# Performance work log

Hardware: AMD Instinct MI355X
Metric: run time of the kernel (lower is better)

Reference implementation:

```python
import jax, jax.numpy as jnp
import numpy as np

B, S, H, D = 4, 2048, 12, 64
HID = H * D  # 768
EPS = 1e-5


def _layer_norm(h, w, b):
    mu = jnp.mean(h, axis=-1, keepdims=True)
    var = jnp.mean((h - mu) ** 2, axis=-1, keepdims=True)
    return w * (h - mu) / jnp.sqrt(var + EPS) + b


def setup_inputs() -> dict:
    key = jax.random.key(0)
    ks = jax.random.split(key, 12)
    sc = 1.0 / np.sqrt(HID)
    inp = {
        "x": jax.random.normal(ks[0], (B, S, HID), jnp.float32),
        "ln1_w": jnp.ones((HID,), jnp.float32),
        "ln1_b": jnp.zeros((HID,), jnp.float32),
        "Wq": jax.random.normal(ks[1], (HID, HID), jnp.float32) * sc,
        "bq": jnp.zeros((HID,), jnp.float32),
        "Wk": jax.random.normal(ks[2], (HID, HID), jnp.float32) * sc,
        "bk": jnp.zeros((HID,), jnp.float32),
        "Wv": jax.random.normal(ks[3], (HID, HID), jnp.float32) * sc,
        "bv": jnp.zeros((HID,), jnp.float32),
        "Wo": jax.random.normal(ks[4], (HID, HID), jnp.float32) * sc,
        "bo": jnp.zeros((HID,), jnp.float32),
        "ln2_w": jnp.ones((HID,), jnp.float32),
        "ln2_b": jnp.zeros((HID,), jnp.float32),
        "W1": jax.random.normal(ks[5], (HID, 4 * HID), jnp.float32) * sc,
        "b1": jnp.zeros((4 * HID,), jnp.float32),
        "W2": jax.random.normal(ks[6], (4 * HID, HID), jnp.float32) * (1.0 / np.sqrt(4 * HID)),
        "b2": jnp.zeros((HID,), jnp.float32),
    }
    return inp


def _split_heads(t):
    # (B, S, H*D) -> (B, H, S, D)
    b, s, _ = t.shape
    return t.reshape(b, s, H, -1).transpose(0, 2, 1, 3)


def _merge_heads(t):
    # (B, H, S, D) -> (B, S, H*D)
    b, h, s, d = t.shape
    return t.transpose(0, 2, 1, 3).reshape(b, s, h * d)


def _attention(h, Wq, bq, Wk, bk, Wv, bv, Wo, bo):
    q = _split_heads(h @ Wq + bq)  # (B,H,S,D)
    k = _split_heads(h @ Wk + bk)
    v = _split_heads(h @ Wv + bv)
    scores = jnp.einsum("bhqd,bhkd->bhqk", q, k) / jnp.sqrt(jnp.asarray(D, h.dtype))
    causal = jnp.tril(jnp.ones((q.shape[2], q.shape[2]), bool))  # (S,S)
    scores = jnp.where(causal, scores, jnp.finfo(scores.dtype).min)
    w = jax.nn.softmax(scores, axis=-1)
    out = jnp.einsum("bhqk,bhkd->bhqd", w, v)
    return _merge_heads(out) @ Wo + bo


def reference(x, ln1_w, ln1_b, Wq, bq, Wk, bk, Wv, bv, Wo, bo, ln2_w, ln2_b, W1, b1, W2, b2):
    # Pre-LN transformer block: x + attn(LN(x)); then x + MLP(LN(x))
    a = _attention(_layer_norm(x, ln1_w, ln1_b), Wq, bq, Wk, bk, Wv, bv, Wo, bo)
    x = x + a
    h = _layer_norm(x, ln2_w, ln2_b)
    m = jax.nn.gelu(h @ W1 + b1, approximate=False) @ W2 + b2
    return x + m
```

## Files before the change

kernel.cpp:

```cpp
#include <hip/hip_runtime.h>
#include <cmath>
#include <stdint.h>

typedef unsigned short u16;
typedef __attribute__((ext_vector_type(8))) short short8;
typedef __attribute__((ext_vector_type(4))) float f32x4;
typedef __attribute__((ext_vector_type(4))) unsigned int u32x4;

#define HID 768
#define FF  3072
#define SEQ 2048
#define NHEAD 12
#define NROWS 8192

__device__ __forceinline__ float bf2f(u16 u){ return __uint_as_float(((unsigned)u)<<16); }
__device__ __forceinline__ u16 f2bf(float f){
  unsigned x = __float_as_uint(f);
  x += 0x7fffu + ((x>>16)&1u);
  return (u16)(x>>16);
}
__device__ __forceinline__ unsigned pack2(float a, float b){
  return (unsigned)f2bf(a) | ((unsigned)f2bf(b) << 16);
}
__device__ __forceinline__ void gload16(const void* g, void* l){
  __builtin_amdgcn_global_load_lds((const __attribute__((address_space(1))) unsigned*)g,
                                   (__attribute__((address_space(3))) unsigned*)l, 16, 0, 0);
}

__global__ __launch_bounds__(256) void wconv(const float* __restrict__ in,
                                             u16* __restrict__ out, int K, int N)
{
  __shared__ float t[32][33];
  const int bk = blockIdx.x*32, bn = blockIdx.y*32;
  const int tn = threadIdx.x & 31, tk = threadIdx.x >> 5;
  #pragma unroll
  for (int j=0;j<4;++j)
    t[tk+8*j][tn] = in[(size_t)(bk+tk+8*j)*N + bn + tn];
  __syncthreads();
  #pragma unroll
  for (int j=0;j<4;++j)
    out[(size_t)(bn+tk+8*j)*K + bk + tn] = f2bf(t[tn][tk+8*j]);
}

__global__ __launch_bounds__(256) void tconv(const u16* __restrict__ in,
                                             u16* __restrict__ out, int K, int N)
{
  __shared__ u16 t[32][34];
  const int bk = blockIdx.x*32, bn = blockIdx.y*32;
  const int tn = threadIdx.x & 31, tk = threadIdx.x >> 5;
  #pragma unroll
  for (int j=0;j<4;++j)
    t[tk+8*j][tn] = in[(size_t)(bk+tk+8*j)*N + bn + tn];
  __syncthreads();
  #pragma unroll
  for (int j=0;j<4;++j)
    out[(size_t)(bn+tk+8*j)*K + bk + tn] = t[tn][tk+8*j];
}

__global__ __launch_bounds__(256) void ln_k(const float* __restrict__ in,
    const float* __restrict__ gw, const float* __restrict__ gb,
    u16* __restrict__ out)
{
  const int row = blockIdx.x*4 + (threadIdx.x>>6);
  const int l = threadIdx.x & 63;
  const float* p = in + (size_t)row*HID;
  float4 v[3];
  float s=0.f, ss=0.f;
  #pragma unroll
  for (int j=0;j<3;++j){
    v[j] = *(const float4*)(p + j*256 + l*4);
    s  += v[j].x + v[j].y + v[j].z + v[j].w;
    ss += v[j].x*v[j].x + v[j].y*v[j].y + v[j].z*v[j].z + v[j].w*v[j].w;
  }
  #pragma unroll
  for (int m=1;m<64;m<<=1){
    s  += __shfl_xor(s,  m, 64);
    ss += __shfl_xor(ss, m, 64);
  }
  const float mu = s * (1.f/768.f);
  const float rstd = rsqrtf(ss*(1.f/768.f) - mu*mu + 1e-5f);
  #pragma unroll
  for (int j=0;j<3;++j){
    const float4 wv = *(const float4*)(gw + j*256 + l*4);
    const float4 bv = *(const float4*)(gb + j*256 + l*4);
    ushort4 o;
    o.x = f2bf((v[j].x-mu)*rstd*wv.x + bv.x);
    o.y = f2bf((v[j].y-mu)*rstd*wv.y + bv.y);
    o.z = f2bf((v[j].z-mu)*rstd*wv.z + bv.z);
    o.w = f2bf((v[j].w-mu)*rstd*wv.w + bv.w);
    *(ushort4*)(out + (size_t)row*HID + j*256 + l*4) = o;
  }
}

template<int MODE>
__global__ __launch_bounds__(256) void gemm_bt(const u16* __restrict__ A,
    const u16* __restrict__ Bt, const float* __restrict__ bias0,
    const float* __restrict__ bias1, const float* __restrict__ bias2,
    const float* __restrict__ res, void* __restrict__ outp,
    int N, int K, long wstride, long ostride)
{
  __shared__ __align__(16) u16 sA[128*32];
  __shared__ __align__(16) u16 sB[128*32];
  const int tid = threadIdx.x, l = tid&63, w = tid>>6;
  const int wr = w>>1, wc = w&1, hi = l>>4, lo = l&15;
  const int bm = blockIdx.x*128, bn = blockIdx.y*128;
  const int z = blockIdx.z;
  const u16* Bz = Bt + (size_t)z * (size_t)wstride;
  const float* bias = (z==0) ? bias0 : ((z==1)? bias1 : bias2);

  const f32x4 zv = {0.f,0.f,0.f,0.f};
  f32x4 acc[4][4];
  #pragma unroll
  for (int i=0;i<4;++i)
    #pragma unroll
    for (int j=0;j<4;++j) acc[i][j] = zv;

  for (int kt=0; kt<K; kt+=32){
    __syncthreads();
    #pragma unroll
    for (int j=0;j<2;++j){
      int c = tid + 256*j;
      int row = c>>2, off = (c&3)*8;
      gload16(A  + (size_t)(bm + row)*K + kt + off, (char*)sA + c*16);
      gload16(Bz + (size_t)(bn + row)*K + kt + off, (char*)sB + c*16);
    }
    __syncthreads();
    short8 af[4], bfv[4];
    #pragma unroll
    for (int i=0;i<4;++i){
      af[i]  = *(const short8*)(sA + (wr*64 + i*16 + lo)*32 + hi*8);
      bfv[i] = *(const short8*)(sB + (wc*64 + i*16 + lo)*32 + hi*8);
    }
    #pragma unroll
    for (int mi=0;mi<4;++mi)
      #pragma unroll
      for (int ni=0;ni<4;++ni)
        acc[mi][ni] = __builtin_amdgcn_mfma_f32_16x16x32_bf16(af[mi], bfv[ni], acc[mi][ni], 0,0,0);
  }

  #pragma unroll
  for (int mi=0;mi<4;++mi)
    #pragma unroll
    for (int ni=0;ni<4;++ni){
      const int r0 = bm + wr*64 + mi*16 + 4*hi;
      const int cc = bn + wc*64 + ni*16 + lo;
      const float bv = bias[cc];
      #pragma unroll
      for (int g=0; g<4; ++g){
        const size_t idx = (size_t)(r0+g)*N + cc;
        float v = acc[mi][ni][g] + bv;
        if (MODE == 0){
          ((u16*)outp + (size_t)z*(size_t)ostride)[idx] = f2bf(v);
        } else if (MODE == 1){
          ((float*)outp)[idx] = res[idx] + v;
        } else {
          float gx = 0.5f*v*(1.f + erff(v*0.70710678118f));
          ((u16*)outp)[idx] = f2bf(gx);
        }
      }
    }
}

__global__ __launch_bounds__(256, 4) void attn_k(const u16* __restrict__ Qm,
                                                 const u16* __restrict__ Km,
                                                 const u16* __restrict__ Vt,
                                                 u16* __restrict__ Om)
{
  __shared__ __align__(16) u16 sK [64*64];
  __shared__ __align__(16) u16 sVT[64*64];
  const int tid = threadIdx.x, l = tid & 63, w = tid >> 6;
  const int hi = l >> 4, lo = l & 15;
  const int idx = blockIdx.x;
  const int qb = 31 - (idx / 48);
  const int bh = idx % 48;
  const int b = bh / NHEAD, h = bh - (bh / NHEAD) * NHEAD;
  const size_t rb = (size_t)b * SEQ;
  const int qw = qb*64 + w*16;

  short8 qf[2];
  #pragma unroll
  for (int ks=0; ks<2; ++ks){
    short8 t = *(const short8*)(Qm + (rb + qw + lo)*HID + h*64 + ks*32 + hi*8);
    #pragma unroll
    for (int i=0;i<8;++i) t[i] = (short)f2bf(bf2f((u16)t[i]) * 0.125f);
    qf[ks] = t;
  }

  const f32x4 zv = {0.f,0.f,0.f,0.f};
  f32x4 oa[4] = {zv, zv, zv, zv};
  float m = -INFINITY, lsum = 0.f;
  const int srcA = (((2*hi)  & 3) << 4) | lo;
  const int srcB = (((2*hi+1)& 3) << 4) | lo;

  for (int t=0; t<=qb; ++t){
    const int kv0 = t*64;
    __syncthreads();
    #pragma unroll
    for (int j=0;j<2;++j){
      int c = tid + 256*j;
      int row = c >> 3;
      int d0 = ((c&7) ^ (row&7))*8;
      gload16(Km + (rb + kv0 + row)*HID + h*64 + d0, (char*)sK + c*16);
    }
    #pragma unroll
    for (int j=0;j<2;++j){
      int c = tid + 256*j;
      int row = c >> 3;
      int k0 = ((c&7) ^ (row&7))*8;
      gload16(Vt + (size_t)(h*64 + row)*NROWS + rb + kv0 + k0, (char*)sVT + c*16);
    }
    __syncthreads();

    f32x4 sc[4] = {zv, zv, zv, zv};
    #pragma unroll
    for (int ks=0;ks<2;++ks){
      #pragma unroll
      for (int ni=0;ni<4;++ni){
        short8 kf = *(const short8*)(sK + (ni*16 + lo)*64 + ((ks*32 + hi*8) ^ ((lo&7)*8)));
        sc[ni] = __builtin_amdgcn_mfma_f32_16x16x32_bf16(kf, qf[ks], sc[ni], 0,0,0);
      }
    }

    if (t == qb){
      #pragma unroll
      for (int ni=0;ni<4;++ni)
        #pragma unroll
        for (int g=0; g<4; ++g){
          int kg = kv0 + ni*16 + 4*hi + g;
          if (kg > qw + lo) sc[ni][g] = -INFINITY;
        }
    }

    float pm = sc[0][0];
    #pragma unroll
    for (int ni=0;ni<4;++ni)
      #pragma unroll
      for (int g=0; g<4; ++g) pm = fmaxf(pm, sc[ni][g]);
    pm = fmaxf(pm, __shfl_xor(pm, 16, 64));
    pm = fmaxf(pm, __shfl_xor(pm, 32, 64));
    const float mnew = fmaxf(m, pm);
    const float alpha = __expf(m - mnew);
    float ps = 0.f;
    #pragma unroll
    for (int ni=0;ni<4;++ni)
      #pragma unroll
      for (int g=0; g<4; ++g){
        float e = __expf(sc[ni][g] - mnew);
        sc[ni][g] = e;
        ps += e;
      }
    ps += __shfl_xor(ps, 16, 64);
    ps += __shfl_xor(ps, 32, 64);
    lsum = lsum*alpha + ps;
    m = mnew;
    #pragma unroll
    for (int nd=0;nd<4;++nd){
      oa[nd][0]*=alpha; oa[nd][1]*=alpha; oa[nd][2]*=alpha; oa[nd][3]*=alpha;
    }

    #pragma unroll
    for (int ks=0;ks<2;++ks){
      unsigned pkA0 = pack2(sc[2*ks  ][0], sc[2*ks  ][1]);
      unsigned pkA1 = pack2(sc[2*ks  ][2], sc[2*ks  ][3]);
      unsigned pkB0 = pack2(sc[2*ks+1][0], sc[2*ks+1][1]);
      unsigned pkB1 = pack2(sc[2*ks+1][2], sc[2*ks+1][3]);
      unsigned a0 = (unsigned)__shfl((int)pkA0, srcA, 64);
      unsigned b0 = (unsigned)__shfl((int)pkB0, srcA, 64);
      unsigned a1 = (unsigned)__shfl((int)pkA1, srcA, 64);
      unsigned b1 = (unsigned)__shfl((int)pkB1, srcA, 64);
      unsigned a2 = (unsigned)__shfl((int)pkA0, srcB, 64);
      unsigned b2 = (unsigned)__shfl((int)pkB0, srcB, 64);
      unsigned a3 = (unsigned)__shfl((int)pkA1, srcB, 64);
      unsigned b3 = (unsigned)__shfl((int)pkB1, srcB, 64);
      union { u32x4 u; short8 s; } pf;
      pf.u = (u32x4){ (hi<2)?a0:b0, (hi<2)?a1:b1, (hi<2)?a2:b2, (hi<2)?a3:b3 };

      #pragma unroll
      for (int nd=0;nd<4;++nd){
        short8 vf = *(const short8*)(sVT + (nd*16 + lo)*64 + ((ks*32 + hi*8) ^ ((lo&7)*8)));
        oa[nd] = __builtin_amdgcn_mfma_f32_16x16x32_bf16(vf, pf.s, oa[nd], 0,0,0);
      }
    }
  }

  const float inv = 1.f / lsum;
  #pragma unroll
  for (int nd=0;nd<4;++nd){
    ushort4 o;
    o.x = f2bf(oa[nd][0]*inv);
    o.y = f2bf(oa[nd][1]*inv);
    o.z = f2bf(oa[nd][2]*inv);
    o.w = f2bf(oa[nd][3]*inv);
    *(ushort4*)(Om + (rb + qw + lo)*HID + h*64 + nd*16 + 4*hi) = o;
  }
}

extern "C" void kernel_launch(void* const* d_in, const int* in_sizes, int n_in,
                              void* d_out, int out_size, void* d_ws, size_t ws_size,
                              hipStream_t stream)
{
  const float* x    = (const float*)d_in[0];
  const float* ln1w = (const float*)d_in[1];
  const float* ln1b = (const float*)d_in[2];
  const float* Wq   = (const float*)d_in[3];
  const float* bq   = (const float*)d_in[4];
  const float* Wk   = (const float*)d_in[5];
  const float* bk   = (const float*)d_in[6];
  const float* Wv   = (const float*)d_in[7];
  const float* bv   = (const float*)d_in[8];
  const float* Wo   = (const float*)d_in[9];
  const float* bo   = (const float*)d_in[10];
  const float* ln2w = (const float*)d_in[11];
  const float* ln2b = (const float*)d_in[12];
  const float* W1   = (const float*)d_in[13];
  const float* b1   = (const float*)d_in[14];
  const float* W2   = (const float*)d_in[15];
  const float* b2   = (const float*)d_in[16];

  u16* wq_t = (u16*)d_ws;
  u16* wk_t = wq_t + 589824;
  u16* wv_t = wk_t + 589824;
  u16* wo_t = wv_t + 589824;
  u16* w1_t = wo_t + 589824;
  u16* w2_t = w1_t + 2359296;
  u16* hbf  = w2_t + 2359296;
  u16* qb_  = hbf + 6291456;
  u16* kb_  = qb_ + 6291456;
  u16* vb_  = kb_ + 6291456;
  u16* atb  = vb_ + 6291456;
  u16* ub   = qb_;
  float* x2 = (float*)(atb + 6291456);

  const size_t need = 102236160ull;
  if (ws_size < need) return;

  dim3 blk(256);
  wconv<<<dim3(24,24), blk, 0, stream>>>(Wq, wq_t, 768, 768);
  wconv<<<dim3(24,24), blk, 0, stream>>>(Wk, wk_t, 768, 768);
  wconv<<<dim3(24,24), blk, 0, stream>>>(Wv, wv_t, 768, 768);
  wconv<<<dim3(24,24), blk, 0, stream>>>(Wo, wo_t, 768, 768);
  wconv<<<dim3(24,96), blk, 0, stream>>>(W1, w1_t, 768, 3072);
  wconv<<<dim3(96,24), blk, 0, stream>>>(W2, w2_t, 3072, 768);

  ln_k<<<2048, blk, 0, stream>>>(x, ln1w, ln1b, hbf);

  gemm_bt<0><<<dim3(64,6,2), blk, 0, stream>>>(hbf, wq_t, bq, bk, bv,
      nullptr, (void*)qb_, 768, 768, 589824L, 6291456L);
  gemm_bt<0><<<dim3(64,6,1), blk, 0, stream>>>(hbf, wv_t, bv, bv, bv,
      nullptr, (void*)vb_, 768, 768, 0L, 0L);
  tconv<<<dim3(256,24), blk, 0, stream>>>(vb_, hbf, 8192, 768);

  attn_k<<<dim3(1536), blk, 0, stream>>>(qb_, kb_, hbf, atb);

  gemm_bt<1><<<dim3(64,6,1), blk, 0, stream>>>(atb, wo_t, bo, bo, bo,
      x, (void*)x2, 768, 768, 0L, 0L);

  ln_k<<<2048, blk, 0, stream>>>(x2, ln2w, ln2b, hbf);

  gemm_bt<2><<<dim3(64,24,1), blk, 0, stream>>>(hbf, w1_t, b1, b1, b1,
      nullptr, (void*)ub, 3072, 768, 0L, 0L);

  gemm_bt<1><<<dim3(64,6,1), blk, 0, stream>>>(ub, w2_t, b2, b2, b2,
      x2, d_out, 768, 3072, 0L, 0L);
}
```

Before: 432.6 us.

## Double-buffer GEMM LDS tiles, merge V projection launch, approximate GELU with tanh

```diff
diff --git a/kernel.cpp b/kernel.cpp
--- a/kernel.cpp
+++ b/kernel.cpp
@@ -99,8 +99,8 @@
     const float* __restrict__ res, void* __restrict__ outp,
     int N, int K, long wstride, long ostride)
 {
-  __shared__ __align__(16) u16 sA[128*32];
-  __shared__ __align__(16) u16 sB[128*32];
+  __shared__ __align__(16) u16 sA[2][128*32];
+  __shared__ __align__(16) u16 sB[2][128*32];
   const int tid = threadIdx.x, l = tid&63, w = tid>>6;
   const int wr = w>>1, wc = w&1, hi = l>>4, lo = l&15;
   const int bm = blockIdx.x*128, bn = blockIdx.y*128;
@@ -108,6 +108,9 @@
   const u16* Bz = Bt + (size_t)z * (size_t)wstride;
   const float* bias = (z==0) ? bias0 : ((z==1)? bias1 : bias2);
 
+  const u16* Arow = A  + (size_t)bm*K;
+  const u16* Brow = Bz + (size_t)bn*K;
+
   const f32x4 zv = {0.f,0.f,0.f,0.f};
   f32x4 acc[4][4];
   #pragma unroll
@@ -115,27 +118,40 @@
     #pragma unroll
     for (int j=0;j<4;++j) acc[i][j] = zv;
 
-  for (int kt=0; kt<K; kt+=32){
-    __syncthreads();
-    #pragma unroll
-    for (int j=0;j<2;++j){
-      int c = tid + 256*j;
-      int row = c>>2, off = (c&3)*8;
-      gload16(A  + (size_t)(bm + row)*K + kt + off, (char*)sA + c*16);
-      gload16(Bz + (size_t)(bn + row)*K + kt + off, (char*)sB + c*16);
-    }
-    __syncthreads();
+  const int r0_ = tid>>2, off_ = (tid&3)*8;
+  const int r1_ = r0_ + 64;
+
+  {
+    gload16(Arow + (size_t)r0_*K + off_, (char*)sA[0] + tid*16);
+    gload16(Brow + (size_t)r0_*K + off_, (char*)sB[0] + tid*16);
+    gload16(Arow + (size_t)r1_*K + off_, (char*)sA[0] + (tid+256)*16);
+    gload16(Brow + (size_t)r1_*K + off_, (char*)sB[0] + (tid+256)*16);
+  }
+  __syncthreads();
+
+  const int NT = K >> 5;
+  int cur = 0;
+  for (int t=0; t<NT; ++t){
+    if (t+1 < NT){
+      const int kt = (t+1) << 5;
+      gload16(Arow + (size_t)r0_*K + kt + off_, (char*)sA[cur^1] + tid*16);
+      gload16(Brow + (size_t)r0_*K + kt + off_, (char*)sB[cur^1] + tid*16);
+      gload16(Arow + (size_t)r1_*K + kt + off_, (char*)sA[cur^1] + (tid+256)*16);
+      gload16(Brow + (size_t)r1_*K + kt + off_, (char*)sB[cur^1] + (tid+256)*16);
+    }
     short8 af[4], bfv[4];
     #pragma unroll
     for (int i=0;i<4;++i){
-      af[i]  = *(const short8*)(sA + (wr*64 + i*16 + lo)*32 + hi*8);
-      bfv[i] = *(const short8*)(sB + (wc*64 + i*16 + lo)*32 + hi*8);
+      af[i]  = *(const short8*)(sA[cur] + (wr*64 + i*16 + lo)*32 + hi*8);
+      bfv[i] = *(const short8*)(sB[cur] + (wc*64 + i*16 + lo)*32 + hi*8);
     }
     #pragma unroll
     for (int mi=0;mi<4;++mi)
       #pragma unroll
       for (int ni=0;ni<4;++ni)
         acc[mi][ni] = __builtin_amdgcn_mfma_f32_16x16x32_bf16(af[mi], bfv[ni], acc[mi][ni], 0,0,0);
+    __syncthreads();
+    cur ^= 1;
   }
 
   #pragma unroll
@@ -154,8 +170,10 @@
         } else if (MODE == 1){
           ((float*)outp)[idx] = res[idx] + v;
         } else {
-          float gx = 0.5f*v*(1.f + erff(v*0.70710678118f));
-          ((u16*)outp)[idx] = f2bf(gx);
+          float u = v*(0.7978845608f + 0.0356774081f*v*v);
+          float e = __expf(2.f*u);
+          float th = 1.f - 2.f/(1.f + e);
+          ((u16*)outp)[idx] = f2bf(0.5f*v*(1.f + th));
         }
       }
     }
@@ -344,10 +362,8 @@
 
   ln_k<<<2048, blk, 0, stream>>>(x, ln1w, ln1b, hbf);
 
-  gemm_bt<0><<<dim3(64,6,2), blk, 0, stream>>>(hbf, wq_t, bq, bk, bv,
+  gemm_bt<0><<<dim3(64,6,3), blk, 0, stream>>>(hbf, wq_t, bq, bk, bv,
       nullptr, (void*)qb_, 768, 768, 589824L, 6291456L);
-  gemm_bt<0><<<dim3(64,6,1), blk, 0, stream>>>(hbf, wv_t, bv, bv, bv,
-      nullptr, (void*)vb_, 768, 768, 0L, 0L);
   tconv<<<dim3(256,24), blk, 0, stream>>>(vb_, hbf, 8192, 768);
 
   attn_k<<<dim3(1536), blk, 0, stream>>>(qb_, kb_, hbf, atb);
```

Result: faster. 384.0 us (-11.2%).
